# Kernel optimization log

Hardware: AMD Instinct MI355X
Metric: run time of the kernel (lower is better)

## Reference

```python
import jax, jax.numpy as jnp
import numpy as np
from jax import lax

N, D_IN, D_H, D_A, N_CLS, K = 50000, 1024, 512, 256, 2, 8


def setup_inputs() -> dict:
    key = jax.random.key(0)
    ks = jax.random.split(key, 13)
    s = 0.02
    return {
        "h": jax.random.normal(ks[0], (1, N, D_IN), dtype=jnp.float32),
        "fc_W": jax.random.normal(ks[1], (D_H, D_IN), dtype=jnp.float32) * s,
        "fc_b": jnp.zeros((D_H,), jnp.float32),
        "att_a_W": jax.random.normal(ks[2], (D_A, D_H), dtype=jnp.float32) * s,
        "att_a_b": jnp.zeros((D_A,), jnp.float32),
        "att_b_W": jax.random.normal(ks[3], (D_A, D_H), dtype=jnp.float32) * s,
        "att_b_b": jnp.zeros((D_A,), jnp.float32),
        "att_c_W": jax.random.normal(ks[4], (1, D_A), dtype=jnp.float32) * s,
        "att_c_b": jnp.zeros((1,), jnp.float32),
        "cls_W": jax.random.normal(ks[5], (N_CLS, D_H), dtype=jnp.float32) * s,
        "cls_b": jnp.zeros((N_CLS,), jnp.float32),
        "inst_W": jax.random.normal(ks[6], (2, D_H), dtype=jnp.float32) * s,
        "inst_b": jnp.zeros((2,), jnp.float32),
        "label": 1,  # one_hot -> [0,1]: inst_eval runs only for classifier index 1
    }


def reference(h, fc_W, fc_b, att_a_W, att_a_b, att_b_W, att_b_b,
              att_c_W, att_c_b, cls_W, cls_b, inst_W, inst_b, label):
    x = jnp.squeeze(h, 0)                               # [N, 1024]
    hh = jax.nn.relu(x @ fc_W.T + fc_b)                 # [N, 512]
    # gated attention: tanh gate * sigmoid gate -> scalar score per instance
    a = jnp.tanh(hh @ att_a_W.T + att_a_b)              # [N, 256]
    b = jax.nn.sigmoid(hh @ att_b_W.T + att_b_b)        # [N, 256]
    A_raw = (a * b) @ att_c_W.T + att_c_b               # [N, 1]
    A = jax.nn.softmax(A_raw, axis=0)                   # softmax over instances

    # instance eval (label==1, subtyping=False -> only classifier index 1)
    scores = A_raw[:, 0]                                # [N]
    _, top_p_ids = lax.top_k(scores, K)
    _, top_n_ids = lax.top_k(-scores, K)
    ids = jnp.concatenate([top_p_ids, top_n_ids])       # [2K]
    inst = hh[ids]                                      # gather [2K, 512]
    logits = inst @ inst_W.T + inst_b                   # [2K, 2]
    targets = jnp.concatenate([jnp.ones((K,), jnp.int32),
                               jnp.zeros((K,), jnp.int32)])
    logp = jax.nn.log_softmax(logits, axis=-1)
    instance_loss = -jnp.mean(jnp.take_along_axis(logp, targets[:, None], axis=1))

    instance_scores = hh @ cls_W.T + cls_b              # [N, 2]
    preds = (instance_scores * A).sum(axis=0) / A.sum(axis=0)  # [2]
    preds = preds[None, :]                              # [1, 2]
    return preds, instance_scores, A_raw, instance_loss
```

## Files before the change

kernel.cpp:

```cpp
#include <hip/hip_runtime.h>
#include <hip/hip_bf16.h>
#include <math.h>

typedef __bf16 bf16_t;
typedef __bf16 bf16x4 __attribute__((ext_vector_type(4)));
typedef __bf16 bf16x8 __attribute__((ext_vector_type(8)));
typedef float  f32x4  __attribute__((ext_vector_type(4)));

#define NROWS 50000

__global__ void k_convert(const float* __restrict__ fcW,
                          const float* __restrict__ aW,
                          const float* __restrict__ bW,
                          const float* __restrict__ clsW,
                          const float* __restrict__ instW,
                          bf16_t* __restrict__ permW1, bf16_t* __restrict__ permB2,
                          bf16_t* __restrict__ clsWb, bf16_t* __restrict__ instWb) {
    int t = blockIdx.x * 256 + threadIdx.x;
    if (t < 131072) {
        float4 v = *(const float4*)(fcW + (long)t * 4);
        int row = t >> 8;
        int k0 = (t & 255) * 4;
        int kt = k0 >> 5, q = (k0 >> 3) & 3, j = k0 & 7;
        bf16_t o[4] = {(bf16_t)v.x, (bf16_t)v.y, (bf16_t)v.z, (bf16_t)v.w};
        *(bf16x4*)(permW1 + kt * 16384 + q * 4096 + row * 8 + j) = *(bf16x4*)o;
    } else if (t < 196608) {
        int t2 = t - 131072;
        int isB = t2 >> 15;
        int f = t2 & 32767;
        float4 v = *(const float4*)(((isB ? bW : aW)) + (long)f * 4);
        int srow = f >> 7;
        int k0 = (f & 127) * 4;
        int kt = k0 >> 5, q = (k0 >> 3) & 3, j = k0 & 7;
        int r = ((srow >> 4) * 2 + isB) * 16 + (srow & 15);
        bf16_t o[4] = {(bf16_t)v.x, (bf16_t)v.y, (bf16_t)v.z, (bf16_t)v.w};
        *(bf16x4*)(permB2 + kt * 16384 + q * 4096 + r * 8 + j) = *(bf16x4*)o;
    } else if (t < 197632) {
        int i = t - 196608;
        clsWb[i] = (bf16_t)clsW[i];
    } else if (t < 198656) {
        int i = t - 197632;
        instWb[i] = (bf16_t)instW[i];
    }
}

__global__ __launch_bounds__(512, 2) void k_fused(
        const float* __restrict__ x,
        const bf16_t* __restrict__ permW1, const bf16_t* __restrict__ permB2,
        const bf16_t* __restrict__ clsWb, const bf16_t* __restrict__ instWb,
        const float* __restrict__ fcb,
        const float* __restrict__ aab, const float* __restrict__ abb,
        const float* __restrict__ acW, const float* __restrict__ acb,
        const float* __restrict__ clsb, const float* __restrict__ instb,
        float* __restrict__ Araw, float* __restrict__ inst,
        float* __restrict__ instLog) {
    __shared__ __align__(16) char smem[149504];
    bf16_t* hhT = (bf16_t*)(smem + 16384);

    const int tid = threadIdx.x;
    const int w = tid >> 6, l = tid & 63, q = l >> 4, li = l & 15;
    const int wr = w >> 2, wc = w & 3;
    const long row0 = (long)blockIdx.x * 128;

    f32x4 acc[4][8];
    #pragma unroll
    for (int a = 0; a < 4; a++)
        #pragma unroll
        for (int c = 0; c < 8; c++) acc[a][c] = (f32x4)0.0f;

    int arow[2], akx[2]; bool av[2];
    #pragma unroll
    for (int j = 0; j < 2; j++) {
        int s = j * 512 + tid;
        arow[j] = s >> 3; akx[j] = s & 7;
        av[j] = (row0 + arow[j]) < NROWS;
    }
    const float* xb = x + row0 * 1024;

    float4 xv[2];
    #pragma unroll
    for (int j = 0; j < 2; j++)
        xv[j] = av[j] ? *(const float4*)(xb + (long)arow[j] * 1024 + akx[j] * 4)
                      : make_float4(0.f, 0.f, 0.f, 0.f);
    #pragma unroll
    for (int j = 0; j < 2; j++) {
        bf16_t o[4] = {(bf16_t)xv[j].x, (bf16_t)xv[j].y, (bf16_t)xv[j].z, (bf16_t)xv[j].w};
        *(bf16x4*)(smem + (akx[j] >> 1) * 2048 + arow[j] * 16 + (akx[j] & 1) * 8) = *(bf16x4*)o;
    }
    #pragma unroll
    for (int j = 0; j < 2; j++)
        xv[j] = av[j] ? *(const float4*)(xb + (long)arow[j] * 1024 + 32 + akx[j] * 4)
                      : make_float4(0.f, 0.f, 0.f, 0.f);
    __syncthreads();

    for (int kt = 0; kt < 32; kt++) {
        const int cur = kt & 1, nxt = cur ^ 1;
        if (kt < 31) {
            #pragma unroll
            for (int j = 0; j < 2; j++) {
                bf16_t o[4] = {(bf16_t)xv[j].x, (bf16_t)xv[j].y, (bf16_t)xv[j].z, (bf16_t)xv[j].w};
                *(bf16x4*)(smem + nxt * 8192 + (akx[j] >> 1) * 2048 + arow[j] * 16 + (akx[j] & 1) * 8) = *(bf16x4*)o;
            }
            int kn = (kt < 30 ? kt + 2 : 31) * 32;
            #pragma unroll
            for (int j = 0; j < 2; j++)
                xv[j] = av[j] ? *(const float4*)(xb + (long)arow[j] * 1024 + kn + akx[j] * 4)
                              : make_float4(0.f, 0.f, 0.f, 0.f);
        }
        const bf16_t* Ab = (const bf16_t*)(smem + cur * 8192);
        const bf16_t* Bg = permW1 + kt * 16384 + q * 4096;
        bf16x8 bfr[8], afr[4];
        #pragma unroll
        for (int tn = 0; tn < 8; tn++)
            bfr[tn] = *(const bf16x8*)(Bg + (wc * 128 + tn * 16 + li) * 8);
        #pragma unroll
        for (int tm = 0; tm < 4; tm++)
            afr[tm] = *(const bf16x8*)(Ab + q * 1024 + (wr * 64 + tm * 16 + li) * 8);
        #pragma unroll
        for (int tm = 0; tm < 4; tm++)
            #pragma unroll
            for (int tn = 0; tn < 8; tn++)
                acc[tm][tn] = __builtin_amdgcn_mfma_f32_16x16x32_bf16(afr[tm], bfr[tn], acc[tm][tn], 0, 0, 0);
        __syncthreads();
    }

    {
        float bias[8];
        #pragma unroll
        for (int tn = 0; tn < 8; tn++) bias[tn] = fcb[wc * 128 + tn * 16 + li];
        #pragma unroll
        for (int tm = 0; tm < 4; tm++)
            #pragma unroll
            for (int tn = 0; tn < 8; tn++)
                #pragma unroll
                for (int r = 0; r < 4; r++) {
                    float v = acc[tm][tn][r] + bias[tn];
                    v = v > 0.f ? v : 0.f;
                    hhT[(wr * 64 + tm * 16 + q * 4 + r) * 520 + wc * 128 + tn * 16 + li] = (bf16_t)v;
                }
    }
    __syncthreads();

    #pragma unroll
    for (int a = 0; a < 4; a++)
        #pragma unroll
        for (int c = 0; c < 8; c++) acc[a][c] = (f32x4)0.0f;
    float c0[4] = {0,0,0,0}, c1[4] = {0,0,0,0}, c2[4] = {0,0,0,0}, c3[4] = {0,0,0,0};

    for (int kt = 0; kt < 16; kt++) {
        const bf16_t* Bg = permB2 + kt * 16384 + q * 4096;
        bf16x8 bfr[8], afr[4];
        #pragma unroll
        for (int tn = 0; tn < 8; tn++)
            bfr[tn] = *(const bf16x8*)(Bg + (wc * 128 + tn * 16 + li) * 8);
        #pragma unroll
        for (int tm = 0; tm < 4; tm++)
            afr[tm] = *(const bf16x8*)(hhT + (wr * 64 + tm * 16 + li) * 520 + kt * 32 + q * 8);
        #pragma unroll
        for (int tm = 0; tm < 4; tm++)
            #pragma unroll
            for (int tn = 0; tn < 8; tn++)
                acc[tm][tn] = __builtin_amdgcn_mfma_f32_16x16x32_bf16(afr[tm], bfr[tn], acc[tm][tn], 0, 0, 0);
        if ((kt >> 2) == wc) {
            bf16x8 w0 = *(const bf16x8*)(clsWb + kt * 32 + q * 8);
            bf16x8 w1 = *(const bf16x8*)(clsWb + 512 + kt * 32 + q * 8);
            bf16x8 w2 = *(const bf16x8*)(instWb + kt * 32 + q * 8);
            bf16x8 w3 = *(const bf16x8*)(instWb + 512 + kt * 32 + q * 8);
            #pragma unroll
            for (int tm = 0; tm < 4; tm++) {
                float s0 = 0.f, s1 = 0.f, s2 = 0.f, s3 = 0.f;
                #pragma unroll
                for (int jj = 0; jj < 8; jj++) {
                    float a = (float)afr[tm][jj];
                    s0 += a * (float)w0[jj];
                    s1 += a * (float)w1[jj];
                    s2 += a * (float)w2[jj];
                    s3 += a * (float)w3[jj];
                }
                c0[tm] += s0; c1[tm] += s1; c2[tm] += s2; c3[tm] += s3;
            }
        }
    }

    float (*apart)[4]      = (float (*)[4])smem;
    float (*cpart)[128][4] = (float (*)[128][4])(smem + 2048);

    float sum_mr[4][4];
    #pragma unroll
    for (int a = 0; a < 4; a++)
        #pragma unroll
        for (int c = 0; c < 4; c++) sum_mr[a][c] = 0.f;
    #pragma unroll
    for (int p = 0; p < 4; p++) {
        int j = (wc * 4 + p) * 16 + li;
        float ab_ = aab[j], bb_ = abb[j], cw = acW[j];
        #pragma unroll
        for (int tm = 0; tm < 4; tm++)
            #pragma unroll
            for (int r = 0; r < 4; r++) {
                float avv = tanhf(acc[tm][2 * p][r] + ab_);
                float bvv = acc[tm][2 * p + 1][r] + bb_;
                bvv = 1.f / (1.f + expf(-bvv));
                sum_mr[tm][r] += avv * bvv * cw;
            }
    }
    #pragma unroll
    for (int tm = 0; tm < 4; tm++)
        #pragma unroll
        for (int r = 0; r < 4; r++) {
            float v = sum_mr[tm][r];
            v += __shfl_xor(v, 1); v += __shfl_xor(v, 2);
            v += __shfl_xor(v, 4); v += __shfl_xor(v, 8);
            if (li == 0) apart[wr * 64 + tm * 16 + q * 4 + r][wc] = v;
        }
    #pragma unroll
    for (int tm = 0; tm < 4; tm++) {
        float v0 = c0[tm], v1 = c1[tm], v2 = c2[tm], v3 = c3[tm];
        v0 += __shfl_xor(v0, 16); v0 += __shfl_xor(v0, 32);
        v1 += __shfl_xor(v1, 16); v1 += __shfl_xor(v1, 32);
        v2 += __shfl_xor(v2, 16); v2 += __shfl_xor(v2, 32);
        v3 += __shfl_xor(v3, 16); v3 += __shfl_xor(v3, 32);
        if (l < 16) {
            float* cp = cpart[wc][wr * 64 + tm * 16 + li];
            cp[0] = v0; cp[1] = v1; cp[2] = v2; cp[3] = v3;
        }
    }
    __syncthreads();

    if (tid < 128) {
        long g = row0 + tid;
        if (g < NROWS) {
            float s = apart[tid][0] + apart[tid][1] + apart[tid][2] + apart[tid][3] + acb[0];
            Araw[g] = s;
            float o0 = clsb[0], o1 = clsb[1], o2 = instb[0], o3 = instb[1];
            #pragma unroll
            for (int k = 0; k < 4; k++) {
                o0 += cpart[k][tid][0]; o1 += cpart[k][tid][1];
                o2 += cpart[k][tid][2]; o3 += cpart[k][tid][3];
            }
            inst[g * 2]     = o0; inst[g * 2 + 1]     = o1;
            instLog[g * 2]  = o2; instLog[g * 2 + 1]  = o3;
        }
    }
}

__global__ void k_topk_part(const float* __restrict__ scores,
                            float* __restrict__ candV, int* __restrict__ candI,
                            float* __restrict__ sums) {
    __shared__ float cv[4096];
    __shared__ int   ci[4096];
    int tid = threadIdx.x;
    int p = blockIdx.x;
    int pass = p & 1, rq = p >> 1;
    if (p == 0 && tid == 0) { sums[0] = 0.f; sums[1] = 0.f; sums[2] = 0.f; }
    float sign = pass ? -1.f : 1.f;
    int lo = rq * 12500, hi = lo + 12500;
    float tv[8]; int ti[8];
    #pragma unroll
    for (int k = 0; k < 8; k++) { tv[k] = -1e30f; ti[k] = 0x7fffffff; }
    for (int i = lo + tid; i < hi; i += 512) {
        float v = sign * scores[i];
        if (v > tv[7] || (v == tv[7] && i < ti[7])) {
            int k = 7;
            while (k > 0 && (v > tv[k-1] || (v == tv[k-1] && i < ti[k-1]))) {
                tv[k] = tv[k-1]; ti[k] = ti[k-1]; k--;
            }
            tv[k] = v; ti[k] = i;
        }
    }
    #pragma unroll
    for (int k = 0; k < 8; k++) { cv[tid * 8 + k] = tv[k]; ci[tid * 8 + k] = ti[k]; }
    __syncthreads();
    if (tid < 64) {
        float mv[8]; int mi[8];
        #pragma unroll
        for (int k = 0; k < 8; k++) { mv[k] = -1e30f; mi[k] = 0x7fffffff; }
        for (int i = 0; i < 64; i++) {
            int slot = tid * 64 + ((i + tid) & 63);
            float v = cv[slot]; int idx = ci[slot];
            #pragma unroll
            for (int k = 0; k < 8; k++) {
                bool bt = (v > mv[k]) || (v == mv[k] && idx < mi[k]);
                float nv = bt ? v : mv[k];  int ni = bt ? idx : mi[k];
                float ov = bt ? mv[k] : v;  int oi = bt ? mi[k] : idx;
                mv[k] = nv; mi[k] = ni; v = ov; idx = oi;
            }
        }
        for (int r = 0; r < 8; r++) {
            float bv = mv[0]; int bi = mi[0]; int bs = tid;
            for (int m = 1; m < 64; m <<= 1) {
                float ov = __shfl_xor(bv, m); int oi = __shfl_xor(bi, m); int os = __shfl_xor(bs, m);
                if (ov > bv || (ov == bv && oi < bi)) { bv = ov; bi = oi; bs = os; }
            }
            if (tid == 0) {
                candV[pass * 32 + rq * 8 + r] = bv;
                candI[pass * 32 + rq * 8 + r] = bi;
            }
            if (tid == bs) {
                #pragma unroll
                for (int k = 0; k < 7; k++) { mv[k] = mv[k+1]; mi[k] = mi[k+1]; }
                mv[7] = -1e30f; mi[7] = 0x7fffffff;
            }
        }
    }
}

__global__ void k_sum(const float* __restrict__ Araw, const float* __restrict__ inst,
                      const float* __restrict__ candV, float* sums) {
    __shared__ float r0[4], r1[4], r2[4];
    int tid = threadIdx.x;
    float mx = -1e30f;
    #pragma unroll
    for (int p = 0; p < 4; p++) mx = fmaxf(mx, candV[p * 8]);
    float se = 0.f, s0 = 0.f, s1 = 0.f;
    for (int i = blockIdx.x * 256 + tid; i < NROWS; i += 32768) {
        float e = expf(Araw[i] - mx);
        se += e; s0 += inst[2 * i] * e; s1 += inst[2 * i + 1] * e;
    }
    for (int s = 1; s < 64; s <<= 1) {
        se += __shfl_xor(se, s); s0 += __shfl_xor(s0, s); s1 += __shfl_xor(s1, s);
    }
    if ((tid & 63) == 0) { r0[tid >> 6] = se; r1[tid >> 6] = s0; r2[tid >> 6] = s1; }
    __syncthreads();
    if (tid == 0) {
        atomicAdd(&sums[0], r0[0] + r0[1] + r0[2] + r0[3]);
        atomicAdd(&sums[1], r1[0] + r1[1] + r1[2] + r1[3]);
        atomicAdd(&sums[2], r2[0] + r2[1] + r2[2] + r2[3]);
    }
}

__global__ void k_fin(const float* __restrict__ instLog,
                      const float* __restrict__ candV, const int* __restrict__ candI,
                      const float* __restrict__ sums, float* __restrict__ dout) {
    __shared__ int mid[16];
    int tid = threadIdx.x;
    int wv = tid >> 6, l = tid & 63;
    if (wv < 2) {
        float v; int idx;
        if (l < 32) { v = candV[wv * 32 + l]; idx = candI[wv * 32 + l]; }
        else        { v = -1e30f; idx = 0x7fffffff; }
        for (int r = 0; r < 8; r++) {
            float bv = v; int bi = idx; int bs = l;
            for (int m = 1; m < 64; m <<= 1) {
                float ov = __shfl_xor(bv, m); int oi = __shfl_xor(bi, m); int os = __shfl_xor(bs, m);
                if (ov > bv || (ov == bv && oi < bi)) { bv = ov; bi = oi; bs = os; }
            }
            if (l == 0) mid[wv * 8 + r] = bi;
            if (l == bs) { v = -1e30f; idx = 0x7fffffff; }
        }
    }
    __syncthreads();
    if (tid < 16) {
        int id = mid[tid];
        float l0 = instLog[id * 2], l1 = instLog[id * 2 + 1];
        float mx = fmaxf(l0, l1);
        float lse = mx + logf(expf(l0 - mx) + expf(l1 - mx));
        float lt = (tid < 8) ? l1 : l0;
        float term = lse - lt;
        for (int m = 1; m < 16; m <<= 1) term += __shfl_xor(term, m);
        if (tid == 0) {
            dout[150002] = term / 16.f;
            float se = sums[0];
            dout[0] = sums[1] / se;
            dout[1] = sums[2] / se;
        }
    }
}

extern "C" void kernel_launch(void* const* d_in, const int* in_sizes, int n_in,
                              void* d_out, int out_size, void* d_ws, size_t ws_size,
                              hipStream_t stream) {
    const float* h   = (const float*)d_in[0];
    const float* fcW = (const float*)d_in[1];
    const float* fcb = (const float*)d_in[2];
    const float* aaW = (const float*)d_in[3];
    const float* aab = (const float*)d_in[4];
    const float* abW = (const float*)d_in[5];
    const float* abb = (const float*)d_in[6];
    const float* acW = (const float*)d_in[7];
    const float* acb = (const float*)d_in[8];
    const float* clW = (const float*)d_in[9];
    const float* clb = (const float*)d_in[10];
    const float* inW = (const float*)d_in[11];
    const float* inb = (const float*)d_in[12];
    float* out = (float*)d_out;

    char* ws = (char*)d_ws;
    bf16_t* permW1  = (bf16_t*)(ws);
    bf16_t* permB2  = (bf16_t*)(ws + 1048576);
    bf16_t* clsWb   = (bf16_t*)(ws + 1572864);
    bf16_t* instWb  = (bf16_t*)(ws + 1574912);
    float*  instLog = (float*) (ws + 1576960);
    float*  candV   = (float*) (ws + 1976960);
    int*    candI   = (int*)   (ws + 1977216);
    float*  sums    = (float*) (ws + 1977472);

    float* inst = out + 2;
    float* Araw = out + 2 + 100000;

    k_convert<<<776, 256, 0, stream>>>(fcW, aaW, abW, clW, inW, permW1, permB2, clsWb, instWb);
    k_fused<<<391, 512, 0, stream>>>(h, permW1, permB2, clsWb, instWb,
                                     fcb, aab, abb, acW, acb, clb, inb,
                                     Araw, inst, instLog);
    k_topk_part<<<8, 512, 0, stream>>>(Araw, candV, candI, sums);
    k_sum<<<128, 256, 0, stream>>>(Araw, inst, candV, sums);
    k_fin<<<1, 128, 0, stream>>>(instLog, candV, candI, sums, out);
}
```

Before: 492.4 us.

## Shrink fused tile to 32 rows, fold cls/inst heads into MFMA, merge reductions

The fused MLP kernel now processes 32 rows per 256-thread block instead of 128 rows per 512 threads. This cuts shared memory from about 146KB to 38KB so more blocks can be resident and the tail imbalance shrinks. The classifier and instance heads are packed as extra columns into the attention weight buffer and computed with MFMA instead of scalar dot products. The fused kernel also writes a global max score through an atomicMax on an order-preserving key, so the softmax-sum and top-k partial kernels can merge into one launch. The cost is that each weight tile is re-read from global or L2 by four times as many blocks.

Measured after the change: 588.3 us. 19.5% more time.

```diff
diff --git a/kernel.cpp b/kernel.cpp
--- a/kernel.cpp
+++ b/kernel.cpp
@@ -8,6 +8,14 @@
 typedef float  f32x4  __attribute__((ext_vector_type(4)));
 
 #define NROWS 50000
+
+__device__ __forceinline__ unsigned int encf(float f) {
+    unsigned int u = __float_as_uint(f);
+    return (u >> 31) ? ~u : (u | 0x80000000u);
+}
+__device__ __forceinline__ float decf(unsigned int u) {
+    return (u >> 31) ? __uint_as_float(u & 0x7fffffffu) : __uint_as_float(~u);
+}
 
 __global__ void k_convert(const float* __restrict__ fcW,
                           const float* __restrict__ aW,
@@ -15,8 +23,12 @@
                           const float* __restrict__ clsW,
                           const float* __restrict__ instW,
                           bf16_t* __restrict__ permW1, bf16_t* __restrict__ permB2,
-                          bf16_t* __restrict__ clsWb, bf16_t* __restrict__ instWb) {
+                          float* __restrict__ sums) {
     int t = blockIdx.x * 256 + threadIdx.x;
+    if (t == 0) {
+        sums[0] = 0.f; sums[1] = 0.f; sums[2] = 0.f;
+        ((unsigned int*)sums)[3] = 0u;
+    }
     if (t < 131072) {
         float4 v = *(const float4*)(fcW + (long)t * 4);
         int row = t >> 8;
@@ -34,298 +46,283 @@
         int kt = k0 >> 5, q = (k0 >> 3) & 3, j = k0 & 7;
         int r = ((srow >> 4) * 2 + isB) * 16 + (srow & 15);
         bf16_t o[4] = {(bf16_t)v.x, (bf16_t)v.y, (bf16_t)v.z, (bf16_t)v.w};
-        *(bf16x4*)(permB2 + kt * 16384 + q * 4096 + r * 8 + j) = *(bf16x4*)o;
-    } else if (t < 197632) {
-        int i = t - 196608;
-        clsWb[i] = (bf16_t)clsW[i];
-    } else if (t < 198656) {
-        int i = t - 197632;
-        instWb[i] = (bf16_t)instW[i];
-    }
-}
-
-__global__ __launch_bounds__(512, 2) void k_fused(
+        *(bf16x4*)(permB2 + kt * 16896 + q * 4224 + r * 8 + j) = *(bf16x4*)o;
+    } else if (t < 197120) {
+        int k = t - 196608;
+        int kt = k >> 5, q = (k >> 3) & 3, j = k & 7;
+        bf16_t* base = permB2 + kt * 16896 + q * 4224 + j;
+        base[(512 + 0) * 8] = (bf16_t)clsW[k];
+        base[(512 + 1) * 8] = (bf16_t)clsW[512 + k];
+        base[(512 + 2) * 8] = (bf16_t)instW[k];
+        base[(512 + 3) * 8] = (bf16_t)instW[512 + k];
+    }
+}
+
+__global__ __launch_bounds__(256, 4) void k_fused(
         const float* __restrict__ x,
         const bf16_t* __restrict__ permW1, const bf16_t* __restrict__ permB2,
-        const bf16_t* __restrict__ clsWb, const bf16_t* __restrict__ instWb,
         const float* __restrict__ fcb,
         const float* __restrict__ aab, const float* __restrict__ abb,
         const float* __restrict__ acW, const float* __restrict__ acb,
         const float* __restrict__ clsb, const float* __restrict__ instb,
         float* __restrict__ Araw, float* __restrict__ inst,
-        float* __restrict__ instLog) {
-    __shared__ __align__(16) char smem[149504];
-    bf16_t* hhT = (bf16_t*)(smem + 16384);
+        float* __restrict__ instLog, unsigned int* __restrict__ maxkey) {
+    __shared__ __align__(16) char smem[38400];
+    bf16_t* hhT = (bf16_t*)(smem + 5120);
 
     const int tid = threadIdx.x;
-    const int w = tid >> 6, l = tid & 63, q = l >> 4, li = l & 15;
-    const int wr = w >> 2, wc = w & 3;
-    const long row0 = (long)blockIdx.x * 128;
-
-    f32x4 acc[4][8];
+    const int wc = tid >> 6, l = tid & 63, q = l >> 4, li = l & 15;
+    const long row0 = (long)blockIdx.x * 32;
+
+    f32x4 acc[2][8];
     #pragma unroll
-    for (int a = 0; a < 4; a++)
+    for (int a = 0; a < 2; a++)
         #pragma unroll
         for (int c = 0; c < 8; c++) acc[a][c] = (f32x4)0.0f;
 
-    int arow[2], akx[2]; bool av[2];
+    const int srow = tid >> 3;
+    const int sk   = (tid & 7) * 4;
+    const bool av  = (row0 + srow) < NROWS;
+    const float* xr = x + (row0 + srow) * 1024 + sk;
+
+    float4 xv = av ? *(const float4*)xr : make_float4(0.f, 0.f, 0.f, 0.f);
+    {
+        bf16_t o[4] = {(bf16_t)xv.x, (bf16_t)xv.y, (bf16_t)xv.z, (bf16_t)xv.w};
+        *(bf16x4*)(smem + srow * 80 + sk * 2) = *(bf16x4*)o;
+    }
+    xv = av ? *(const float4*)(xr + 32) : make_float4(0.f, 0.f, 0.f, 0.f);
+    __syncthreads();
+
+    for (int kt = 0; kt < 32; kt++) {
+        const int cur = kt & 1;
+        if (kt < 31) {
+            bf16_t o[4] = {(bf16_t)xv.x, (bf16_t)xv.y, (bf16_t)xv.z, (bf16_t)xv.w};
+            *(bf16x4*)(smem + (cur ^ 1) * 2560 + srow * 80 + sk * 2) = *(bf16x4*)o;
+            if (kt < 30)
+                xv = av ? *(const float4*)(xr + (kt + 2) * 32) : make_float4(0.f, 0.f, 0.f, 0.f);
+        }
+        const char* As = smem + cur * 2560;
+        const bf16_t* Bg = permW1 + kt * 16384 + q * 4096;
+        bf16x8 afr[2], bfrA[4], bfrB[4];
+        #pragma unroll
+        for (int tn = 0; tn < 4; tn++)
+            bfrA[tn] = *(const bf16x8*)(Bg + (wc * 128 + tn * 16 + li) * 8);
+        #pragma unroll
+        for (int tn = 0; tn < 4; tn++)
+            bfrB[tn] = *(const bf16x8*)(Bg + (wc * 128 + (tn + 4) * 16 + li) * 8);
+        #pragma unroll
+        for (int tm = 0; tm < 2; tm++)
+            afr[tm] = *(const bf16x8*)(As + (tm * 16 + li) * 80 + q * 16);
+        #pragma unroll
+        for (int tm = 0; tm < 2; tm++)
+            #pragma unroll
+            for (int tn = 0; tn < 4; tn++)
+                acc[tm][tn] = __builtin_amdgcn_mfma_f32_16x16x32_bf16(afr[tm], bfrA[tn], acc[tm][tn], 0, 0, 0);
+        #pragma unroll
+        for (int tm = 0; tm < 2; tm++)
+            #pragma unroll
+            for (int tn = 0; tn < 4; tn++)
+                acc[tm][tn + 4] = __builtin_amdgcn_mfma_f32_16x16x32_bf16(afr[tm], bfrB[tn], acc[tm][tn + 4], 0, 0, 0);
+        __syncthreads();
+    }
+
     #pragma unroll
-    for (int j = 0; j < 2; j++) {
-        int s = j * 512 + tid;
-        arow[j] = s >> 3; akx[j] = s & 7;
-        av[j] = (row0 + arow[j]) < NROWS;
-    }
-    const float* xb = x + row0 * 1024;
-
-    float4 xv[2];
+    for (int tn = 0; tn < 8; tn++) {
+        float bias = fcb[wc * 128 + tn * 16 + li];
+        #pragma unroll
+        for (int tm = 0; tm < 2; tm++)
+            #pragma unroll
+            for (int r = 0; r < 4; r++) {
+                float v = acc[tm][tn][r] + bias;
+                v = v > 0.f ? v : 0.f;
+                hhT[(tm * 16 + q * 4 + r) * 520 + wc * 128 + tn * 16 + li] = (bf16_t)v;
+            }
+    }
+    __syncthreads();
+
+    float (*apart)[4] = (float (*)[4])smem;
+    float (*cpart)[4] = (float (*)[4])(smem + 512);
+
+    float sum_mr[2][4];
     #pragma unroll
-    for (int j = 0; j < 2; j++)
-        xv[j] = av[j] ? *(const float4*)(xb + (long)arow[j] * 1024 + akx[j] * 4)
-                      : make_float4(0.f, 0.f, 0.f, 0.f);
+    for (int a = 0; a < 2; a++)
+        #pragma unroll
+        for (int c = 0; c < 4; c++) sum_mr[a][c] = 0.f;
+
     #pragma unroll
-    for (int j = 0; j < 2; j++) {
-        bf16_t o[4] = {(bf16_t)xv[j].x, (bf16_t)xv[j].y, (bf16_t)xv[j].z, (bf16_t)xv[j].w};
-        *(bf16x4*)(smem + (akx[j] >> 1) * 2048 + arow[j] * 16 + (akx[j] & 1) * 8) = *(bf16x4*)o;
-    }
-    #pragma unroll
-    for (int j = 0; j < 2; j++)
-        xv[j] = av[j] ? *(const float4*)(xb + (long)arow[j] * 1024 + 32 + akx[j] * 4)
-                      : make_float4(0.f, 0.f, 0.f, 0.f);
-    __syncthreads();
-
-    for (int kt = 0; kt < 32; kt++) {
-        const int cur = kt & 1, nxt = cur ^ 1;
-        if (kt < 31) {
-            #pragma unroll
-            for (int j = 0; j < 2; j++) {
-                bf16_t o[4] = {(bf16_t)xv[j].x, (bf16_t)xv[j].y, (bf16_t)xv[j].z, (bf16_t)xv[j].w};
-                *(bf16x4*)(smem + nxt * 8192 + (akx[j] >> 1) * 2048 + arow[j] * 16 + (akx[j] & 1) * 8) = *(bf16x4*)o;
-            }
-            int kn = (kt < 30 ? kt + 2 : 31) * 32;
-            #pragma unroll
-            for (int j = 0; j < 2; j++)
-                xv[j] = av[j] ? *(const float4*)(xb + (long)arow[j] * 1024 + kn + akx[j] * 4)
-                              : make_float4(0.f, 0.f, 0.f, 0.f);
-        }
-        const bf16_t* Ab = (const bf16_t*)(smem + cur * 8192);
-        const bf16_t* Bg = permW1 + kt * 16384 + q * 4096;
-        bf16x8 bfr[8], afr[4];
-        #pragma unroll
-        for (int tn = 0; tn < 8; tn++)
-            bfr[tn] = *(const bf16x8*)(Bg + (wc * 128 + tn * 16 + li) * 8);
-        #pragma unroll
-        for (int tm = 0; tm < 4; tm++)
-            afr[tm] = *(const bf16x8*)(Ab + q * 1024 + (wr * 64 + tm * 16 + li) * 8);
-        #pragma unroll
-        for (int tm = 0; tm < 4; tm++)
-            #pragma unroll
-            for (int tn = 0; tn < 8; tn++)
-                acc[tm][tn] = __builtin_amdgcn_mfma_f32_16x16x32_bf16(afr[tm], bfr[tn], acc[tm][tn], 0, 0, 0);
-        __syncthreads();
-    }
-
-    {
-        float bias[8];
-        #pragma unroll
-        for (int tn = 0; tn < 8; tn++) bias[tn] = fcb[wc * 128 + tn * 16 + li];
-        #pragma unroll
-        for (int tm = 0; tm < 4; tm++)
-            #pragma unroll
-            for (int tn = 0; tn < 8; tn++)
+    for (int p = 0; p < 2; p++) {
+        f32x4 acc2[2][4];
+        #pragma unroll
+        for (int a = 0; a < 2; a++)
+            #pragma unroll
+            for (int c = 0; c < 4; c++) acc2[a][c] = (f32x4)0.0f;
+        f32x4 ax[2];
+        if (p == 0) { ax[0] = (f32x4)0.0f; ax[1] = (f32x4)0.0f; }
+
+        for (int kt = 0; kt < 16; kt++) {
+            const bf16_t* Bg = permB2 + kt * 16896 + q * 4224;
+            bf16x8 bfr[4], afr2[2];
+            #pragma unroll
+            for (int tn = 0; tn < 4; tn++)
+                bfr[tn] = *(const bf16x8*)(Bg + (p * 256 + wc * 64 + tn * 16 + li) * 8);
+            #pragma unroll
+            for (int tm = 0; tm < 2; tm++)
+                afr2[tm] = *(const bf16x8*)(hhT + (tm * 16 + li) * 520 + kt * 32 + q * 8);
+            #pragma unroll
+            for (int tm = 0; tm < 2; tm++)
+                #pragma unroll
+                for (int tn = 0; tn < 4; tn++)
+                    acc2[tm][tn] = __builtin_amdgcn_mfma_f32_16x16x32_bf16(afr2[tm], bfr[tn], acc2[tm][tn], 0, 0, 0);
+            if (p == 0) {
+                bf16x8 bx = *(const bf16x8*)(Bg + (512 + li) * 8);
+                #pragma unroll
+                for (int tm = 0; tm < 2; tm++)
+                    ax[tm] = __builtin_amdgcn_mfma_f32_16x16x32_bf16(afr2[tm], bx, ax[tm], 0, 0, 0);
+            }
+        }
+
+        #pragma unroll
+        for (int pp = 0; pp < 2; pp++) {
+            int j = (p * 8 + wc * 2 + pp) * 16 + li;
+            float ab_ = aab[j], bb_ = abb[j], cw = acW[j];
+            #pragma unroll
+            for (int tm = 0; tm < 2; tm++)
                 #pragma unroll
                 for (int r = 0; r < 4; r++) {
-                    float v = acc[tm][tn][r] + bias[tn];
-                    v = v > 0.f ? v : 0.f;
-                    hhT[(wr * 64 + tm * 16 + q * 4 + r) * 520 + wc * 128 + tn * 16 + li] = (bf16_t)v;
-                }
-    }
-    __syncthreads();
+                    float avv = tanhf(acc2[tm][2 * pp][r] + ab_);
+                    float bvv = acc2[tm][2 * pp + 1][r] + bb_;
+                    bvv = 1.f / (1.f + expf(-bvv));
+                    sum_mr[tm][r] += avv * bvv * cw;
+                }
+        }
+        if (p == 0 && wc == 0 && li < 4) {
+            #pragma unroll
+            for (int tm = 0; tm < 2; tm++)
+                #pragma unroll
+                for (int r = 0; r < 4; r++)
+                    cpart[tm * 16 + q * 4 + r][li] = ax[tm][r];
+        }
+    }
 
     #pragma unroll
-    for (int a = 0; a < 4; a++)
-        #pragma unroll
-        for (int c = 0; c < 8; c++) acc[a][c] = (f32x4)0.0f;
-    float c0[4] = {0,0,0,0}, c1[4] = {0,0,0,0}, c2[4] = {0,0,0,0}, c3[4] = {0,0,0,0};
-
-    for (int kt = 0; kt < 16; kt++) {
-        const bf16_t* Bg = permB2 + kt * 16384 + q * 4096;
-        bf16x8 bfr[8], afr[4];
-        #pragma unroll
-        for (int tn = 0; tn < 8; tn++)
-            bfr[tn] = *(const bf16x8*)(Bg + (wc * 128 + tn * 16 + li) * 8);
-        #pragma unroll
-        for (int tm = 0; tm < 4; tm++)
-            afr[tm] = *(const bf16x8*)(hhT + (wr * 64 + tm * 16 + li) * 520 + kt * 32 + q * 8);
-        #pragma unroll
-        for (int tm = 0; tm < 4; tm++)
-            #pragma unroll
-            for (int tn = 0; tn < 8; tn++)
-                acc[tm][tn] = __builtin_amdgcn_mfma_f32_16x16x32_bf16(afr[tm], bfr[tn], acc[tm][tn], 0, 0, 0);
-        if ((kt >> 2) == wc) {
-            bf16x8 w0 = *(const bf16x8*)(clsWb + kt * 32 + q * 8);
-            bf16x8 w1 = *(const bf16x8*)(clsWb + 512 + kt * 32 + q * 8);
-            bf16x8 w2 = *(const bf16x8*)(instWb + kt * 32 + q * 8);
-            bf16x8 w3 = *(const bf16x8*)(instWb + 512 + kt * 32 + q * 8);
-            #pragma unroll
-            for (int tm = 0; tm < 4; tm++) {
-                float s0 = 0.f, s1 = 0.f, s2 = 0.f, s3 = 0.f;
-                #pragma unroll
-                for (int jj = 0; jj < 8; jj++) {
-                    float a = (float)afr[tm][jj];
-                    s0 += a * (float)w0[jj];
-                    s1 += a * (float)w1[jj];
-                    s2 += a * (float)w2[jj];
-                    s3 += a * (float)w3[jj];
-                }
-                c0[tm] += s0; c1[tm] += s1; c2[tm] += s2; c3[tm] += s3;
-            }
-        }
-    }
-
-    float (*apart)[4]      = (float (*)[4])smem;
-    float (*cpart)[128][4] = (float (*)[128][4])(smem + 2048);
-
-    float sum_mr[4][4];
-    #pragma unroll
-    for (int a = 0; a < 4; a++)
-        #pragma unroll
-        for (int c = 0; c < 4; c++) sum_mr[a][c] = 0.f;
-    #pragma unroll
-    for (int p = 0; p < 4; p++) {
-        int j = (wc * 4 + p) * 16 + li;
-        float ab_ = aab[j], bb_ = abb[j], cw = acW[j];
-        #pragma unroll
-        for (int tm = 0; tm < 4; tm++)
-            #pragma unroll
-            for (int r = 0; r < 4; r++) {
-                float avv = tanhf(acc[tm][2 * p][r] + ab_);
-                float bvv = acc[tm][2 * p + 1][r] + bb_;
-                bvv = 1.f / (1.f + expf(-bvv));
-                sum_mr[tm][r] += avv * bvv * cw;
-            }
-    }
-    #pragma unroll
-    for (int tm = 0; tm < 4; tm++)
+    for (int tm = 0; tm < 2; tm++)
         #pragma unroll
         for (int r = 0; r < 4; r++) {
             float v = sum_mr[tm][r];
             v += __shfl_xor(v, 1); v += __shfl_xor(v, 2);
             v += __shfl_xor(v, 4); v += __shfl_xor(v, 8);
-            if (li == 0) apart[wr * 64 + tm * 16 + q * 4 + r][wc] = v;
-        }
-    #pragma unroll
-    for (int tm = 0; tm < 4; tm++) {
-        float v0 = c0[tm], v1 = c1[tm], v2 = c2[tm], v3 = c3[tm];
-        v0 += __shfl_xor(v0, 16); v0 += __shfl_xor(v0, 32);
-        v1 += __shfl_xor(v1, 16); v1 += __shfl_xor(v1, 32);
-        v2 += __shfl_xor(v2, 16); v2 += __shfl_xor(v2, 32);
-        v3 += __shfl_xor(v3, 16); v3 += __shfl_xor(v3, 32);
-        if (l < 16) {
-            float* cp = cpart[wc][wr * 64 + tm * 16 + li];
-            cp[0] = v0; cp[1] = v1; cp[2] = v2; cp[3] = v3;
-        }
-    }
+            if (li == 0) apart[tm * 16 + q * 4 + r][wc] = v;
+        }
     __syncthreads();
 
-    if (tid < 128) {
+    if (tid < 32) {
         long g = row0 + tid;
+        float s = apart[tid][0] + apart[tid][1] + apart[tid][2] + apart[tid][3] + acb[0];
+        float sv = (g < NROWS) ? s : -3e38f;
         if (g < NROWS) {
-            float s = apart[tid][0] + apart[tid][1] + apart[tid][2] + apart[tid][3] + acb[0];
             Araw[g] = s;
-            float o0 = clsb[0], o1 = clsb[1], o2 = instb[0], o3 = instb[1];
-            #pragma unroll
-            for (int k = 0; k < 4; k++) {
-                o0 += cpart[k][tid][0]; o1 += cpart[k][tid][1];
-                o2 += cpart[k][tid][2]; o3 += cpart[k][tid][3];
-            }
-            inst[g * 2]     = o0; inst[g * 2 + 1]     = o1;
-            instLog[g * 2]  = o2; instLog[g * 2 + 1]  = o3;
-        }
-    }
-}
-
-__global__ void k_topk_part(const float* __restrict__ scores,
-                            float* __restrict__ candV, int* __restrict__ candI,
-                            float* __restrict__ sums) {
-    __shared__ float cv[4096];
-    __shared__ int   ci[4096];
+            inst[g * 2]     = cpart[tid][0] + clsb[0];
+            inst[g * 2 + 1] = cpart[tid][1] + clsb[1];
+            instLog[g * 2]     = cpart[tid][2] + instb[0];
+            instLog[g * 2 + 1] = cpart[tid][3] + instb[1];
+        }
+        unsigned int key = encf(sv);
+        #pragma unroll
+        for (int m = 1; m < 32; m <<= 1) {
+            unsigned int o = __shfl_xor(key, m);
+            key = (o > key) ? o : key;
+        }
+        if (tid == 0) atomicMax(maxkey, key);
+    }
+}
+
+__global__ void k_part(const float* __restrict__ Araw, const float* __restrict__ inst,
+                       float* __restrict__ candV, int* __restrict__ candI,
+                       float* __restrict__ sums) {
+    __shared__ __align__(16) char sm[32768];
     int tid = threadIdx.x;
-    int p = blockIdx.x;
-    int pass = p & 1, rq = p >> 1;
-    if (p == 0 && tid == 0) { sums[0] = 0.f; sums[1] = 0.f; sums[2] = 0.f; }
-    float sign = pass ? -1.f : 1.f;
-    int lo = rq * 12500, hi = lo + 12500;
-    float tv[8]; int ti[8];
-    #pragma unroll
-    for (int k = 0; k < 8; k++) { tv[k] = -1e30f; ti[k] = 0x7fffffff; }
-    for (int i = lo + tid; i < hi; i += 512) {
-        float v = sign * scores[i];
-        if (v > tv[7] || (v == tv[7] && i < ti[7])) {
-            int k = 7;
-            while (k > 0 && (v > tv[k-1] || (v == tv[k-1] && i < ti[k-1]))) {
-                tv[k] = tv[k-1]; ti[k] = ti[k-1]; k--;
-            }
-            tv[k] = v; ti[k] = i;
-        }
-    }
-    #pragma unroll
-    for (int k = 0; k < 8; k++) { cv[tid * 8 + k] = tv[k]; ci[tid * 8 + k] = ti[k]; }
-    __syncthreads();
-    if (tid < 64) {
-        float mv[8]; int mi[8];
-        #pragma unroll
-        for (int k = 0; k < 8; k++) { mv[k] = -1e30f; mi[k] = 0x7fffffff; }
-        for (int i = 0; i < 64; i++) {
-            int slot = tid * 64 + ((i + tid) & 63);
-            float v = cv[slot]; int idx = ci[slot];
-            #pragma unroll
-            for (int k = 0; k < 8; k++) {
-                bool bt = (v > mv[k]) || (v == mv[k] && idx < mi[k]);
-                float nv = bt ? v : mv[k];  int ni = bt ? idx : mi[k];
-                float ov = bt ? mv[k] : v;  int oi = bt ? mi[k] : idx;
-                mv[k] = nv; mi[k] = ni; v = ov; idx = oi;
-            }
-        }
-        for (int r = 0; r < 8; r++) {
-            float bv = mv[0]; int bi = mi[0]; int bs = tid;
-            for (int m = 1; m < 64; m <<= 1) {
-                float ov = __shfl_xor(bv, m); int oi = __shfl_xor(bi, m); int os = __shfl_xor(bs, m);
-                if (ov > bv || (ov == bv && oi < bi)) { bv = ov; bi = oi; bs = os; }
-            }
-            if (tid == 0) {
-                candV[pass * 32 + rq * 8 + r] = bv;
-                candI[pass * 32 + rq * 8 + r] = bi;
-            }
-            if (tid == bs) {
+    int b = blockIdx.x;
+    if (b < 8) {
+        float* cv = (float*)sm;
+        int*   ci = (int*)(sm + 16384);
+        int pass = b & 1, rq = b >> 1;
+        float sign = pass ? -1.f : 1.f;
+        int lo = rq * 12500, hi = lo + 12500;
+        float tv[8]; int ti[8];
+        #pragma unroll
+        for (int k = 0; k < 8; k++) { tv[k] = -1e30f; ti[k] = 0x7fffffff; }
+        for (int i = lo + tid; i < hi; i += 512) {
+            float v = sign * Araw[i];
+            if (v > tv[7] || (v == tv[7] && i < ti[7])) {
+                int k = 7;
+                while (k > 0 && (v > tv[k-1] || (v == tv[k-1] && i < ti[k-1]))) {
+                    tv[k] = tv[k-1]; ti[k] = ti[k-1]; k--;
+                }
+                tv[k] = v; ti[k] = i;
+            }
+        }
+        #pragma unroll
+        for (int k = 0; k < 8; k++) { cv[tid * 8 + k] = tv[k]; ci[tid * 8 + k] = ti[k]; }
+        __syncthreads();
+        if (tid < 64) {
+            float mv[8]; int mi[8];
+            #pragma unroll
+            for (int k = 0; k < 8; k++) { mv[k] = -1e30f; mi[k] = 0x7fffffff; }
+            for (int i = 0; i < 64; i++) {
+                int slot = tid * 64 + ((i + tid) & 63);
+                float v = cv[slot]; int idx = ci[slot];
                 #pragma unroll
-                for (int k = 0; k < 7; k++) { mv[k] = mv[k+1]; mi[k] = mi[k+1]; }
-                mv[7] = -1e30f; mi[7] = 0x7fffffff;
-            }
-        }
-    }
-}
-
-__global__ void k_sum(const float* __restrict__ Araw, const float* __restrict__ inst,
-                      const float* __restrict__ candV, float* sums) {
-    __shared__ float r0[4], r1[4], r2[4];
-    int tid = threadIdx.x;
-    float mx = -1e30f;
-    #pragma unroll
-    for (int p = 0; p < 4; p++) mx = fmaxf(mx, candV[p * 8]);
-    float se = 0.f, s0 = 0.f, s1 = 0.f;
-    for (int i = blockIdx.x * 256 + tid; i < NROWS; i += 32768) {
-        float e = expf(Araw[i] - mx);
-        se += e; s0 += inst[2 * i] * e; s1 += inst[2 * i + 1] * e;
-    }
-    for (int s = 1; s < 64; s <<= 1) {
-        se += __shfl_xor(se, s); s0 += __shfl_xor(s0, s); s1 += __shfl_xor(s1, s);
-    }
-    if ((tid & 63) == 0) { r0[tid >> 6] = se; r1[tid >> 6] = s0; r2[tid >> 6] = s1; }
-    __syncthreads();
-    if (tid == 0) {
-        atomicAdd(&sums[0], r0[0] + r0[1] + r0[2] + r0[3]);
-        atomicAdd(&sums[1], r1[0] + r1[1] + r1[2] + r1[3]);
-        atomicAdd(&sums[2], r2[0] + r2[1] + r2[2] + r2[3]);
+                for (int k = 0; k < 8; k++) {
+                    bool bt = (v > mv[k]) || (v == mv[k] && idx < mi[k]);
+                    float nv = bt ? v : mv[k];  int ni = bt ? idx : mi[k];
+                    float ov = bt ? mv[k] : v;  int oi = bt ? mi[k] : idx;
+                    mv[k] = nv; mi[k] = ni; v = ov; idx = oi;
+                }
+            }
+            for (int r = 0; r < 8; r++) {
+                float bv = mv[0]; int bi = mi[0]; int bs = tid;
+                for (int m = 1; m < 64; m <<= 1) {
+                    float ov = __shfl_xor(bv, m); int oi = __shfl_xor(bi, m); int os = __shfl_xor(bs, m);
+                    if (ov > bv || (ov == bv && oi < bi)) { bv = ov; bi = oi; bs = os; }
+                }
+                if (tid == 0) {
+                    candV[pass * 32 + rq * 8 + r] = bv;
+                    candI[pass * 32 + rq * 8 + r] = bi;
+                }
+                if (tid == bs) {
+                    #pragma unroll
+                    for (int k = 0; k < 7; k++) { mv[k] = mv[k+1]; mi[k] = mi[k+1]; }
+                    mv[7] = -1e30f; mi[7] = 0x7fffffff;
+                }
+            }
+        }
+    } else {
+        float* r0 = (float*)sm;
+        float* r1 = r0 + 8;
+        float* r2 = r0 + 16;
+        float mx = decf(((const unsigned int*)sums)[3]);
+        int i = (b - 8) * 512 + tid;
+        float se = 0.f, s0 = 0.f, s1 = 0.f;
+        if (i < NROWS) {
+            float e = expf(Araw[i] - mx);
+            se = e; s0 = inst[2 * i] * e; s1 = inst[2 * i + 1] * e;
+        }
+        for (int s = 1; s < 64; s <<= 1) {
+            se += __shfl_xor(se, s); s0 += __shfl_xor(s0, s); s1 += __shfl_xor(s1, s);
+        }
+        int w = tid >> 6;
+        if ((tid & 63) == 0) { r0[w] = se; r1[w] = s0; r2[w] = s1; }
+        __syncthreads();
+        if (tid == 0) {
+            float a0 = 0.f, a1 = 0.f, a2 = 0.f;
+            #pragma unroll
+            for (int k = 0; k < 8; k++) { a0 += r0[k]; a1 += r1[k]; a2 += r2[k]; }
+            if (a0 != 0.f || a1 != 0.f || a2 != 0.f) {
+                atomicAdd(&sums[0], a0);
+                atomicAdd(&sums[1], a1);
+                atomicAdd(&sums[2], a2);
+            }
+        }
     }
 }
 
@@ -388,21 +385,17 @@
     char* ws = (char*)d_ws;
     bf16_t* permW1  = (bf16_t*)(ws);
     bf16_t* permB2  = (bf16_t*)(ws + 1048576);
-    bf16_t* clsWb   = (bf16_t*)(ws + 1572864);
-    bf16_t* instWb  = (bf16_t*)(ws + 1574912);
-    float*  instLog = (float*) (ws + 1576960);
-    float*  candV   = (float*) (ws + 1976960);
-    int*    candI   = (int*)   (ws + 1977216);
-    float*  sums    = (float*) (ws + 1977472);
+    float*  instLog = (float*) (ws + 1589248);
+    float*  candV   = (float*) (ws + 1989248);
+    int*    candI   = (int*)   (ws + 1989504);
+    float*  sums    = (float*) (ws + 1989760);
 
     float* inst = out + 2;
     float* Araw = out + 2 + 100000;
 
-    k_convert<<<776, 256, 0, stream>>>(fcW, aaW, abW, clW, inW, permW1, permB2, clsWb, instWb);
-    k_fused<<<391, 512, 0, stream>>>(h, permW1, permB2, clsWb, instWb,
-                                     fcb, aab, abb, acW, acb, clb, inb,
-                                     Araw, inst, instLog);
-    k_topk_part<<<8, 512, 0, stream>>>(Araw, candV, candI, sums);
-    k_sum<<<128, 256, 0, stream>>>(Araw, inst, candV, sums);
+    k_convert<<<770, 256, 0, stream>>>(fcW, aaW, abW, clW, inW, permW1, permB2, sums);
+    k_fused<<<1563, 256, 0, stream>>>(h, permW1, permB2, fcb, aab, abb, acW, acb, clb, inb,
+                                      Araw, inst, instLog, (unsigned int*)sums + 3);
+    k_part<<<136, 512, 0, stream>>>(Araw, inst, candV, candI, sums);
     k_fin<<<1, 128, 0, stream>>>(instLog, candV, candI, sums, out);
 }
```
